# Optimization experiments

Measured on AMD Instinct MI355X. Metric: run time of the kernel, lower is better.

## Reference

```python
import jax, jax.numpy as jnp
import numpy as np

E, S, D_IN, D_LAT, D_HID = 1024, 64, 128, 128, 512
NSTEPS, DT = 8192, 0.01
KL_WEIGHT = 0.01


def setup_inputs() -> dict:
    key = jax.random.key(0)
    ks = jax.random.split(key, 12)
    sd = lambda fan_in: 1.0 / np.sqrt(fan_in)
    return {
        'event_marks': jax.random.normal(ks[0], (E, D_IN), jnp.float32),
        'z_events': jax.random.normal(ks[1], (E, S, D_LAT), jnp.float32),
        'z_traj': jax.random.normal(ks[2], (NSTEPS, S, D_LAT), jnp.float32),
        'times': jnp.arange(NSTEPS + 1, dtype=jnp.float32) * DT,
        'Wp': jax.random.normal(ks[3], (D_IN, D_LAT), jnp.float32) * sd(D_IN),
        'bp': jnp.zeros((D_LAT,), jnp.float32),
        'W1': jax.random.normal(ks[4], (D_LAT, D_HID), jnp.float32) * sd(D_LAT),
        'b1': jnp.zeros((D_HID,), jnp.float32),
        'W2': jax.random.normal(ks[5], (D_HID, 1), jnp.float32) * sd(D_HID),
        'b2': jnp.zeros((1,), jnp.float32),
        'base_intensity': jnp.asarray(0.1, jnp.float32),
        'Wd1': jax.random.normal(ks[6], (D_LAT, D_HID), jnp.float32) * sd(D_LAT),
        'bd1': jnp.zeros((D_HID,), jnp.float32),
        'Wd2': jax.random.normal(ks[7], (D_HID, D_LAT), jnp.float32) * sd(D_HID),
        'bd2': jnp.zeros((D_LAT,), jnp.float32),
    }


def reference(event_marks, z_events, z_traj, times, Wp, bp, W1, b1, W2, b2,
              base_intensity, Wd1, bd1, Wd2, bd2):
    # input projection of marks: [E, D_LAT]
    marks_proj = event_marks @ Wp + bp

    def intensity(z):  # z: [..., D_LAT] -> [...]
        h = jax.nn.relu(z @ W1 + b1)
        s = (h @ W2 + b2)[..., 0]
        return jax.nn.softplus(s + base_intensity)

    # log-intensity at events: sum over events of mean over samples
    lam_ev = intensity(z_events)                      # [E, S]
    log_intensity_sum = jnp.log(lam_ev + 1e-8).mean(axis=1).sum()

    # compensator integral over the trajectory (left Riemann sum)
    lam_traj = intensity(z_traj)                      # [NSTEPS, S]
    dts = jnp.diff(times)                             # [NSTEPS]
    integral = (lam_traj.mean(axis=1) * dts).sum()

    # Gaussian decoder log-prob: mu = MLP(z), unit variance
    h = jax.nn.relu(z_events @ Wd1 + bd1)             # [E, S, D_HID]
    mu = h @ Wd2 + bd2                                # [E, S, D_LAT]
    x = marks_proj[:, None, :]                        # [E, 1, D_LAT]
    log_2pi = jnp.log(jnp.asarray(2.0 * np.pi, jnp.float32))
    log_p = -0.5 * jnp.sum((x - mu) ** 2, axis=-1) - 0.5 * D_LAT * log_2pi  # [E, S]
    recon_loss = log_p.mean(axis=1).sum()

    kl_loss = KL_WEIGHT * jnp.mean(z_traj ** 2)

    elbo = log_intensity_sum - integral + recon_loss - kl_loss
    return -elbo
```

## Files before the change

kernel.cpp:

```cpp
#include <hip/hip_runtime.h>

typedef __attribute__((ext_vector_type(4))) float f32x4;
typedef __attribute__((ext_vector_type(8))) __bf16 bf16x8;
typedef __attribute__((ext_vector_type(4))) __bf16 bf16x4;

#define LOG_2PI 1.8378770664093453f

__device__ __forceinline__ float softplus_f(float x) {
  return fmaxf(x, 0.f) + log1pf(expf(-fabsf(x)));
}

__device__ __forceinline__ void barrier_lds_only() {
  asm volatile("s_waitcnt lgkmcnt(0)\n\ts_barrier" ::: "memory");
}

__global__ void prep_kernel(const float* __restrict__ em,
                            const float* __restrict__ Wp,
                            const float* __restrict__ bp,
                            float* __restrict__ mp,
                            float* __restrict__ accs) {
  const int b = blockIdx.x;
  if (b == 1024) {
    if (threadIdx.x < 8) accs[threadIdx.x] = 0.f;
    return;
  }
  const int d = threadIdx.x;
  float s = bp[d];
  const float* emr = em + b * 128;
#pragma unroll 4
  for (int k = 0; k < 128; ++k) s += emr[k] * Wp[k * 128 + d];
  mp[b * 128 + d] = s;
}

__global__ __launch_bounds__(768, 3) void intensity8_kernel(
    const float* __restrict__ z_traj, const float* __restrict__ z_ev,
    const float* __restrict__ W1, const float* __restrict__ b1,
    const float* __restrict__ W2, const float* __restrict__ b2,
    const float* __restrict__ base_i, const float* __restrict__ times,
    float* __restrict__ accs) {
  __shared__ __align__(16) __bf16 w1t[512 * 128];
  __shared__ __align__(16) float b1L[512];
  __shared__ __align__(16) float w2L[512];
  __shared__ float red[12][4];

  const int tid = threadIdx.x;
  const int wid = tid >> 6, lid = tid & 63;
  const int g = lid >> 4, q = lid & 15;

  if (tid < 512) {
    const float* wcol = W1 + tid;
    char* wb = (char*)w1t;
    const int colbase = tid * 256;
    const int sw = (tid & 7) << 4;
#pragma unroll 8
    for (int k = 0; k < 128; k += 2) {
      float a = wcol[(size_t)k * 512];
      float c = wcol[(size_t)(k + 1) * 512];
      union { __bf16 h[2]; unsigned u; } pk;
      pk.h[0] = (__bf16)a;
      pk.h[1] = (__bf16)c;
      *(unsigned*)(wb + (colbase + ((k * 2) ^ sw))) = pk.u;
    }
    b1L[tid] = b1[tid];
    w2L[tid] = W2[tid];
  }
  const float sbias = b2[0] + base_i[0];
  barrier_lds_only();

  const int gw = blockIdx.x * 12 + wid;
  float integral_loc = 0.f, logsum_loc = 0.f, kls = 0.f;
  const char* wb = (const char*)w1t;
  const int wsw = (q & 7) << 4;

#pragma unroll 1
  for (int p = gw; p < 9216; p += 3072) {
    const bool traj_p = (p < 8192);
    const float* zbase = traj_p ? (z_traj + (size_t)p * 8192)
                                : (z_ev + (size_t)(p - 8192) * 8192);

    bf16x8 fr[4][4];
#pragma unroll
    for (int s = 0; s < 4; ++s) {
      const float* rp = zbase + (s * 16 + q) * 128 + g * 8;
      f32x4 ld[4][2];
#pragma unroll
      for (int kf = 0; kf < 4; ++kf) {
        ld[kf][0] = *(const f32x4*)(rp + kf * 32);
        ld[kf][1] = *(const f32x4*)(rp + kf * 32 + 4);
      }
#pragma unroll
      for (int kf = 0; kf < 4; ++kf) {
        f32x4 a0 = ld[kf][0], a1 = ld[kf][1];
        if (traj_p) {
          kls += a0[0] * a0[0] + a0[1] * a0[1] + a0[2] * a0[2] + a0[3] * a0[3];
          kls += a1[0] * a1[0] + a1[1] * a1[1] + a1[2] * a1[2] + a1[3] * a1[3];
        }
        bf16x8 f;
#pragma unroll
        for (int j = 0; j < 4; ++j) {
          f[j] = (__bf16)a0[j];
          f[4 + j] = (__bf16)a1[j];
        }
        fr[s][kf] = f;
      }
    }

    float rowacc0 = 0.f, rowacc1 = 0.f, rowacc2 = 0.f, rowacc3 = 0.f;
#pragma unroll 2
    for (int c = 0; c < 32; ++c) {
      f32x4 a0 = {}, a1 = {}, a2 = {}, a3 = {};
#pragma unroll
      for (int kf = 0; kf < 4; ++kf) {
        bf16x8 wf = *(const bf16x8*)(wb + c * 4096 + q * 256 +
                                     ((kf * 64 + g * 16) ^ wsw));
        a0 = __builtin_amdgcn_mfma_f32_16x16x32_bf16(wf, fr[0][kf], a0, 0, 0, 0);
        a1 = __builtin_amdgcn_mfma_f32_16x16x32_bf16(wf, fr[1][kf], a1, 0, 0, 0);
        a2 = __builtin_amdgcn_mfma_f32_16x16x32_bf16(wf, fr[2][kf], a2, 0, 0, 0);
        a3 = __builtin_amdgcn_mfma_f32_16x16x32_bf16(wf, fr[3][kf], a3, 0, 0, 0);
      }
      f32x4 bb = *(const f32x4*)&b1L[c * 16 + g * 4];
      f32x4 ww = *(const f32x4*)&w2L[c * 16 + g * 4];
#pragma unroll
      for (int ii = 0; ii < 4; ++ii) {
        rowacc0 += fmaxf(a0[ii] + bb[ii], 0.f) * ww[ii];
        rowacc1 += fmaxf(a1[ii] + bb[ii], 0.f) * ww[ii];
        rowacc2 += fmaxf(a2[ii] + bb[ii], 0.f) * ww[ii];
        rowacc3 += fmaxf(a3[ii] + bb[ii], 0.f) * ww[ii];
      }
    }
    rowacc0 += __shfl_xor(rowacc0, 16);
    rowacc0 += __shfl_xor(rowacc0, 32);
    rowacc1 += __shfl_xor(rowacc1, 16);
    rowacc1 += __shfl_xor(rowacc1, 32);
    rowacc2 += __shfl_xor(rowacc2, 16);
    rowacc2 += __shfl_xor(rowacc2, 32);
    rowacc3 += __shfl_xor(rowacc3, 16);
    rowacc3 += __shfl_xor(rowacc3, 32);

    {
      const int s = lid >> 4;
      const float rs = (s == 0) ? rowacc0 : (s == 1) ? rowacc1
                     : (s == 2) ? rowacc2 : rowacc3;
      const float lam = softplus_f(rs + sbias);
      if (traj_p) {
        integral_loc += lam * (times[p + 1] - times[p]) * (1.f / 64.f);
      } else {
        logsum_loc += logf(lam + 1e-8f) * (1.f / 64.f);
      }
    }
  }

#pragma unroll
  for (int m = 32; m >= 1; m >>= 1) {
    integral_loc += __shfl_xor(integral_loc, m);
    logsum_loc += __shfl_xor(logsum_loc, m);
    kls += __shfl_xor(kls, m);
  }
  if (lid == 0) {
    red[wid][0] = integral_loc;
    red[wid][1] = logsum_loc;
    red[wid][2] = kls;
  }
  __syncthreads();
  if (tid == 0) {
    float I = 0.f, L = 0.f, K = 0.f;
#pragma unroll
    for (int w = 0; w < 12; ++w) {
      I += red[w][0];
      L += red[w][1];
      K += red[w][2];
    }
    atomicAdd(&accs[0], I);
    atomicAdd(&accs[1], L);
    atomicAdd(&accs[3], K);
  }
}

__global__ __launch_bounds__(512, 2) void decoder2_kernel(
    const float* __restrict__ z,
    const float* __restrict__ Wd1, const float* __restrict__ bd1,
    const float* __restrict__ Wd2, const float* __restrict__ bd2,
    const float* __restrict__ mp, float* __restrict__ recon_acc) {
  __shared__ __align__(16) __bf16 zbuf[2][32 * 128];
  __shared__ __align__(16) __bf16 hbuf[32 * 512];
  __shared__ float s_part[32][9];
  __shared__ float red[8];

  const int tid = threadIdx.x;
  const int wid = tid >> 6, lid = tid & 63;
  const int g = lid >> 4, q = lid & 15;
  const int cb = wid * 64;
  const int tile0 = blockIdx.x * 4;

  bf16x8 bw1[4][4];
  f32x4 bd1v[4];
#pragma unroll
  for (int cf = 0; cf < 4; ++cf) {
    const int col = cb + cf * 16 + q;
#pragma unroll
    for (int i = 0; i < 4; ++i) bd1v[cf][i] = bd1[cb + cf * 16 + g * 4 + i];
#pragma unroll
    for (int kf = 0; kf < 4; ++kf) {
      bf16x8 f;
#pragma unroll
      for (int j = 0; j < 8; ++j) f[j] = (__bf16)Wd1[(kf * 32 + g * 8 + j) * 512 + col];
      bw1[cf][kf] = f;
    }
  }
  const int dimf = wid * 16 + q;
  bf16x8 bw2[16];
#pragma unroll
  for (int kf2 = 0; kf2 < 16; ++kf2) {
    bf16x8 f;
#pragma unroll
    for (int j = 0; j < 8; ++j) f[j] = (__bf16)Wd2[(kf2 * 32 + g * 8 + j) * 128 + dimf];
    bw2[kf2] = f;
  }
  f32x4 bd2v;
#pragma unroll
  for (int i = 0; i < 4; ++i) bd2v[i] = bd2[wid * 16 + g * 4 + i];

  const int srow = tid >> 4, sk8 = (tid & 15) * 8;
  const int stg_byte = ((srow * 256 + sk8 * 2) ^ ((srow & 7) << 4));
  char* hb = (char*)hbuf;

  float local = 0.f;

  {
    const float* p = z + (size_t)tile0 * 4096 + tid * 8;
    f32x4 r0 = *(const f32x4*)p, r1 = *(const f32x4*)(p + 4);
    bf16x8 v;
#pragma unroll
    for (int j = 0; j < 4; ++j) { v[j] = (__bf16)r0[j]; v[4 + j] = (__bf16)r1[j]; }
    *(bf16x8*)((char*)zbuf[0] + stg_byte) = v;
  }
  f32x4 rA0, rA1, rB0, rB1;
  { const float* p = z + (size_t)(tile0 + 1) * 4096 + tid * 8; rA0 = *(const f32x4*)p; rA1 = *(const f32x4*)(p + 4); }
  { const float* p = z + (size_t)(tile0 + 2) * 4096 + tid * 8; rB0 = *(const f32x4*)p; rB1 = *(const f32x4*)(p + 4); }
  barrier_lds_only();

#define DBODY(T, ZC, RR0, RR1)                                                     \
  do {                                                                             \
    f32x4 acc1[2][4] = {};                                                         \
    char* zc = (char*)zbuf[ZC];                                                    \
    _Pragma("unroll") for (int kf = 0; kf < 4; ++kf) {                             \
      _Pragma("unroll") for (int rf = 0; rf < 2; ++rf) {                           \
        const int row = rf * 16 + q;                                               \
        bf16x8 a = *(const bf16x8*)(zc + ((row * 256 + kf * 64 + g * 16) ^ ((row & 7) << 4))); \
        _Pragma("unroll") for (int cf = 0; cf < 4; ++cf)                           \
          acc1[rf][cf] = __builtin_amdgcn_mfma_f32_16x16x32_bf16(bw1[cf][kf], a, acc1[rf][cf], 0, 0, 0); \
      }                                                                            \
    }                                                                              \
    {                                                                              \
      bf16x8 v;                                                                    \
      _Pragma("unroll") for (int j = 0; j < 4; ++j) { v[j] = (__bf16)RR0[j]; v[4 + j] = (__bf16)RR1[j]; } \
      *(bf16x8*)((char*)zbuf[(ZC) ^ 1] + stg_byte) = v;                            \
    }                                                                              \
    {                                                                              \
      int tl = (T) + 3; if (tl > 3) tl = 3;                                        \
      const float* p = z + (size_t)(tile0 + tl) * 4096 + tid * 8;                  \
      RR0 = *(const f32x4*)p; RR1 = *(const f32x4*)(p + 4);                        \
    }                                                                              \
    _Pragma("unroll") for (int rf = 0; rf < 2; ++rf) {                             \
      const int row = rf * 16 + q;                                                 \
      _Pragma("unroll") for (int cf = 0; cf < 4; ++cf) {                           \
        bf16x4 hv;                                                                 \
        _Pragma("unroll") for (int i = 0; i < 4; ++i)                              \
          hv[i] = (__bf16)fmaxf(acc1[rf][cf][i] + bd1v[cf][i], 0.f);               \
        const int byt = ((row * 1024 + (cb + cf * 16 + g * 4) * 2) ^ ((row & 7) << 4)); \
        *(bf16x4*)(hb + byt) = hv;                                                 \
      }                                                                            \
    }                                                                              \
    barrier_lds_only();                                                            \
    f32x4 acc2[2] = {};                                                            \
    _Pragma("unroll") for (int kf2 = 0; kf2 < 16; ++kf2) {                         \
      _Pragma("unroll") for (int rf2 = 0; rf2 < 2; ++rf2) {                        \
        const int row = rf2 * 16 + q;                                              \
        bf16x8 a = *(const bf16x8*)(hb + ((row * 1024 + kf2 * 64 + g * 16) ^ ((row & 7) << 4))); \
        acc2[rf2] = __builtin_amdgcn_mfma_f32_16x16x32_bf16(bw2[kf2], a, acc2[rf2], 0, 0, 0); \
      }                                                                            \
    }                                                                              \
    const int e = (tile0 + (T)) >> 1;                                              \
    _Pragma("unroll") for (int rf2 = 0; rf2 < 2; ++rf2) {                          \
      float partial = 0.f;                                                         \
      _Pragma("unroll") for (int i = 0; i < 4; ++i) {                              \
        const float xv = mp[e * 128 + wid * 16 + g * 4 + i];                       \
        const float d = xv - (acc2[rf2][i] + bd2v[i]);                             \
        partial += d * d;                                                          \
      }                                                                            \
      partial += __shfl_xor(partial, 16);                                          \
      partial += __shfl_xor(partial, 32);                                          \
      if (lid < 16) s_part[rf2 * 16 + lid][wid] = partial;                         \
    }                                                                              \
    barrier_lds_only();                                                            \
    if (tid < 32) {                                                                \
      float t2 = 0.f;                                                              \
      _Pragma("unroll") for (int w = 0; w < 8; ++w) t2 += s_part[tid][w];          \
      local += (-0.5f * t2 - 0.5f * 128.f * LOG_2PI) * (1.f / 64.f);               \
    }                                                                              \
  } while (0)

#pragma unroll 1
  for (int t = 0; t < 4; t += 2) {
    DBODY(t, 0, rA0, rA1);
    DBODY(t + 1, 1, rB0, rB1);
  }
#undef DBODY

  if (wid == 0) {
#pragma unroll
    for (int m = 16; m >= 1; m >>= 1) local += __shfl_xor(local, m);
    if (lid == 0) atomicAdd(recon_acc, local);
  }
}

__global__ void finalize_kernel(const float* __restrict__ accs, float* __restrict__ out) {
  const float kl = 0.01f * (accs[3] / 67108864.f);
  const float elbo = accs[1] - accs[0] + accs[2] - kl;
  out[0] = -elbo;
}

extern "C" void kernel_launch(void* const* d_in, const int* in_sizes, int n_in,
                              void* d_out, int out_size, void* d_ws, size_t ws_size,
                              hipStream_t stream) {
  const float* event_marks = (const float*)d_in[0];
  const float* z_events = (const float*)d_in[1];
  const float* z_traj = (const float*)d_in[2];
  const float* times = (const float*)d_in[3];
  const float* Wp = (const float*)d_in[4];
  const float* bp = (const float*)d_in[5];
  const float* W1 = (const float*)d_in[6];
  const float* b1 = (const float*)d_in[7];
  const float* W2 = (const float*)d_in[8];
  const float* b2 = (const float*)d_in[9];
  const float* base_i = (const float*)d_in[10];
  const float* Wd1 = (const float*)d_in[11];
  const float* bd1 = (const float*)d_in[12];
  const float* Wd2 = (const float*)d_in[13];
  const float* bd2 = (const float*)d_in[14];

  float* mp = (float*)d_ws;
  float* accs = (float*)((char*)d_ws + 1024 * 128 * 4);

  prep_kernel<<<1025, 128, 0, stream>>>(event_marks, Wp, bp, mp, accs);
  intensity8_kernel<<<256, 768, 0, stream>>>(z_traj, z_events, W1, b1, W2, b2,
                                             base_i, times, accs);
  decoder2_kernel<<<512, 512, 0, stream>>>(z_events, Wd1, bd1, Wd2, bd2, mp,
                                           &accs[2]);
  finalize_kernel<<<1, 1, 0, stream>>>(accs, (float*)d_out);
}
```

Measured before the change: 148.3 us.

## Prefetch next z tile into registers while computing current intensity tile

The intensity kernel drops from 12 to 8 waves per block, and the work is remapped so each wave handles four trajectory tiles plus an event tile on alternate waves. Registers are double-buffered so the next tile's global loads are issued before the MFMA loop on the current tile. The first tile's load is also issued before the W1 staging into LDS, hiding that latency. The cost is 32 extra f32x4 registers per lane, fewer resident waves, and an uneven 5-versus-4 round split across waves.

Measured after the change: 187.5 us. 26.5% more time.

```diff
diff --git a/kernel.cpp b/kernel.cpp
--- a/kernel.cpp
+++ b/kernel.cpp
@@ -32,7 +32,7 @@
   mp[b * 128 + d] = s;
 }
 
-__global__ __launch_bounds__(768, 3) void intensity8_kernel(
+__global__ __launch_bounds__(512, 2) void intensity9_kernel(
     const float* __restrict__ z_traj, const float* __restrict__ z_ev,
     const float* __restrict__ W1, const float* __restrict__ b1,
     const float* __restrict__ W2, const float* __restrict__ b2,
@@ -41,15 +41,34 @@
   __shared__ __align__(16) __bf16 w1t[512 * 128];
   __shared__ __align__(16) float b1L[512];
   __shared__ __align__(16) float w2L[512];
-  __shared__ float red[12][4];
+  __shared__ float red[8][4];
 
   const int tid = threadIdx.x;
   const int wid = tid >> 6, lid = tid & 63;
   const int g = lid >> 4, q = lid & 15;
-
-  if (tid < 512) {
+  const int gw = blockIdx.x * 8 + wid;
+  const int nrounds = (gw & 1) ? 4 : 5;
+
+  f32x4 stg[4][4][2];
+
+#define ZPTR(P) ((P) < 8192 ? z_traj + (size_t)(P) * 8192 \
+                            : z_ev + (size_t)((P) - 8192) * 8192)
+#define LOADP(ZP)                                                          \
+  do {                                                                     \
+    _Pragma("unroll") for (int s = 0; s < 4; ++s) {                        \
+      const float* rp = (ZP) + (s * 16 + q) * 128 + g * 8;                 \
+      _Pragma("unroll") for (int kf = 0; kf < 4; ++kf) {                   \
+        stg[s][kf][0] = *(const f32x4*)(rp + kf * 32);                     \
+        stg[s][kf][1] = *(const f32x4*)(rp + kf * 32 + 4);                 \
+      }                                                                    \
+    }                                                                      \
+  } while (0)
+
+  LOADP(ZPTR(gw));
+
+  {
     const float* wcol = W1 + tid;
-    char* wb = (char*)w1t;
+    char* wbs = (char*)w1t;
     const int colbase = tid * 256;
     const int sw = (tid & 7) << 4;
 #pragma unroll 8
@@ -59,7 +78,7 @@
       union { __bf16 h[2]; unsigned u; } pk;
       pk.h[0] = (__bf16)a;
       pk.h[1] = (__bf16)c;
-      *(unsigned*)(wb + (colbase + ((k * 2) ^ sw))) = pk.u;
+      *(unsigned*)(wbs + (colbase + ((k * 2) ^ sw))) = pk.u;
     }
     b1L[tid] = b1[tid];
     w2L[tid] = W2[tid];
@@ -67,31 +86,22 @@
   const float sbias = b2[0] + base_i[0];
   barrier_lds_only();
 
-  const int gw = blockIdx.x * 12 + wid;
   float integral_loc = 0.f, logsum_loc = 0.f, kls = 0.f;
   const char* wb = (const char*)w1t;
   const int wsw = (q & 7) << 4;
 
 #pragma unroll 1
-  for (int p = gw; p < 9216; p += 3072) {
-    const bool traj_p = (p < 8192);
-    const float* zbase = traj_p ? (z_traj + (size_t)p * 8192)
-                                : (z_ev + (size_t)(p - 8192) * 8192);
+  for (int r = 0; r < nrounds; ++r) {
+    const bool traj_r = (r < 4);
+    const int p = traj_r ? r * 2048 + gw : 8192 + (gw >> 1);
 
     bf16x8 fr[4][4];
 #pragma unroll
     for (int s = 0; s < 4; ++s) {
-      const float* rp = zbase + (s * 16 + q) * 128 + g * 8;
-      f32x4 ld[4][2];
 #pragma unroll
       for (int kf = 0; kf < 4; ++kf) {
-        ld[kf][0] = *(const f32x4*)(rp + kf * 32);
-        ld[kf][1] = *(const f32x4*)(rp + kf * 32 + 4);
-      }
-#pragma unroll
-      for (int kf = 0; kf < 4; ++kf) {
-        f32x4 a0 = ld[kf][0], a1 = ld[kf][1];
-        if (traj_p) {
+        f32x4 a0 = stg[s][kf][0], a1 = stg[s][kf][1];
+        if (traj_r) {
           kls += a0[0] * a0[0] + a0[1] * a0[1] + a0[2] * a0[2] + a0[3] * a0[3];
           kls += a1[0] * a1[0] + a1[1] * a1[1] + a1[2] * a1[2] + a1[3] * a1[3];
         }
@@ -104,6 +114,13 @@
         fr[s][kf] = f;
       }
     }
+
+    if (r + 1 < nrounds) {
+      const int pn = (r + 1 < 4) ? (r + 1) * 2048 + gw : 8192 + (gw >> 1);
+      const float* zn = ZPTR(pn);
+      LOADP(zn);
+    }
+    __builtin_amdgcn_sched_barrier(0);
 
     float rowacc0 = 0.f, rowacc1 = 0.f, rowacc2 = 0.f, rowacc3 = 0.f;
 #pragma unroll 2
@@ -142,13 +159,15 @@
       const float rs = (s == 0) ? rowacc0 : (s == 1) ? rowacc1
                      : (s == 2) ? rowacc2 : rowacc3;
       const float lam = softplus_f(rs + sbias);
-      if (traj_p) {
+      if (traj_r) {
         integral_loc += lam * (times[p + 1] - times[p]) * (1.f / 64.f);
       } else {
         logsum_loc += logf(lam + 1e-8f) * (1.f / 64.f);
       }
     }
   }
+#undef LOADP
+#undef ZPTR
 
 #pragma unroll
   for (int m = 32; m >= 1; m >>= 1) {
@@ -165,7 +184,7 @@
   if (tid == 0) {
     float I = 0.f, L = 0.f, K = 0.f;
 #pragma unroll
-    for (int w = 0; w < 12; ++w) {
+    for (int w = 0; w < 8; ++w) {
       I += red[w][0];
       L += red[w][1];
       K += red[w][2];
@@ -343,7 +362,7 @@
   float* accs = (float*)((char*)d_ws + 1024 * 128 * 4);
 
   prep_kernel<<<1025, 128, 0, stream>>>(event_marks, Wp, bp, mp, accs);
-  intensity8_kernel<<<256, 768, 0, stream>>>(z_traj, z_events, W1, b1, W2, b2,
+  intensity9_kernel<<<256, 512, 0, stream>>>(z_traj, z_events, W1, b1, W2, b2,
                                              base_i, times, accs);
   decoder2_kernel<<<512, 512, 0, stream>>>(z_events, Wd1, bd1, Wd2, bd2, mp,
                                            &accs[2]);
```

## Fuse mark projection into intensity kernel, fold bias into MFMA, halve decoder tiles

Applied to the files above, without the earlier changes.

Removes the separate prep kernel: the marks projection now runs in 171 extra blocks appended to the intensity kernel's grid, and the accumulators are zeroed with a memset. In the intensity loop the b1 bias is used as the MFMA accumulator's initial value, and b1/W2 are read from global memory instead of LDS. The decoder now handles 2 tiles per block over 1024 blocks, dropping the multi-tile prefetch pipeline for more parallelism. The aim is less launch overhead and better occupancy, at the cost of losing prefetch overlap in the decoder and adding global loads in the hot loop.

Result: slower. 176.3 us (+18.9%).

```diff
diff --git a/kernel.cpp b/kernel.cpp
--- a/kernel.cpp
+++ b/kernel.cpp
@@ -14,42 +14,39 @@
   asm volatile("s_waitcnt lgkmcnt(0)\n\ts_barrier" ::: "memory");
 }
 
-__global__ void prep_kernel(const float* __restrict__ em,
-                            const float* __restrict__ Wp,
-                            const float* __restrict__ bp,
-                            float* __restrict__ mp,
-                            float* __restrict__ accs) {
-  const int b = blockIdx.x;
-  if (b == 1024) {
-    if (threadIdx.x < 8) accs[threadIdx.x] = 0.f;
-    return;
-  }
-  const int d = threadIdx.x;
-  float s = bp[d];
-  const float* emr = em + b * 128;
-#pragma unroll 4
-  for (int k = 0; k < 128; ++k) s += emr[k] * Wp[k * 128 + d];
-  mp[b * 128 + d] = s;
-}
-
-__global__ __launch_bounds__(768, 3) void intensity8_kernel(
+__global__ __launch_bounds__(768, 3) void intensity13_kernel(
     const float* __restrict__ z_traj, const float* __restrict__ z_ev,
     const float* __restrict__ W1, const float* __restrict__ b1,
     const float* __restrict__ W2, const float* __restrict__ b2,
     const float* __restrict__ base_i, const float* __restrict__ times,
+    const float* __restrict__ em, const float* __restrict__ Wp,
+    const float* __restrict__ bp, float* __restrict__ mp,
     float* __restrict__ accs) {
   __shared__ __align__(16) __bf16 w1t[512 * 128];
-  __shared__ __align__(16) float b1L[512];
-  __shared__ __align__(16) float w2L[512];
   __shared__ float red[12][4];
 
   const int tid = threadIdx.x;
+
+  if (blockIdx.x >= 256) {
+    const int e = (blockIdx.x - 256) * 6 + (tid >> 7);
+    if (e < 1024) {
+      const int d = tid & 127;
+      float s = bp[d];
+      const float* emr = em + e * 128;
+#pragma unroll 4
+      for (int k = 0; k < 128; ++k) s += emr[k] * Wp[k * 128 + d];
+      mp[e * 128 + d] = s;
+    }
+    return;
+  }
+
   const int wid = tid >> 6, lid = tid & 63;
   const int g = lid >> 4, q = lid & 15;
+  const int gw = blockIdx.x * 12 + wid;
 
   if (tid < 512) {
     const float* wcol = W1 + tid;
-    char* wb = (char*)w1t;
+    char* wbs = (char*)w1t;
     const int colbase = tid * 256;
     const int sw = (tid & 7) << 4;
 #pragma unroll 8
@@ -59,15 +56,12 @@
       union { __bf16 h[2]; unsigned u; } pk;
       pk.h[0] = (__bf16)a;
       pk.h[1] = (__bf16)c;
-      *(unsigned*)(wb + (colbase + ((k * 2) ^ sw))) = pk.u;
-    }
-    b1L[tid] = b1[tid];
-    w2L[tid] = W2[tid];
+      *(unsigned*)(wbs + (colbase + ((k * 2) ^ sw))) = pk.u;
+    }
   }
   const float sbias = b2[0] + base_i[0];
   barrier_lds_only();
 
-  const int gw = blockIdx.x * 12 + wid;
   float integral_loc = 0.f, logsum_loc = 0.f, kls = 0.f;
   const char* wb = (const char*)w1t;
   const int wsw = (q & 7) << 4;
@@ -108,7 +102,10 @@
     float rowacc0 = 0.f, rowacc1 = 0.f, rowacc2 = 0.f, rowacc3 = 0.f;
 #pragma unroll 2
     for (int c = 0; c < 32; ++c) {
-      f32x4 a0 = {}, a1 = {}, a2 = {}, a3 = {};
+      const int c0 = c * 16 + g * 4;
+      f32x4 bb = *(const f32x4*)&b1[c0];
+      f32x4 ww = *(const f32x4*)&W2[c0];
+      f32x4 a0 = bb, a1 = bb, a2 = bb, a3 = bb;
 #pragma unroll
       for (int kf = 0; kf < 4; ++kf) {
         bf16x8 wf = *(const bf16x8*)(wb + c * 4096 + q * 256 +
@@ -118,14 +115,12 @@
         a2 = __builtin_amdgcn_mfma_f32_16x16x32_bf16(wf, fr[2][kf], a2, 0, 0, 0);
         a3 = __builtin_amdgcn_mfma_f32_16x16x32_bf16(wf, fr[3][kf], a3, 0, 0, 0);
       }
-      f32x4 bb = *(const f32x4*)&b1L[c * 16 + g * 4];
-      f32x4 ww = *(const f32x4*)&w2L[c * 16 + g * 4];
 #pragma unroll
       for (int ii = 0; ii < 4; ++ii) {
-        rowacc0 += fmaxf(a0[ii] + bb[ii], 0.f) * ww[ii];
-        rowacc1 += fmaxf(a1[ii] + bb[ii], 0.f) * ww[ii];
-        rowacc2 += fmaxf(a2[ii] + bb[ii], 0.f) * ww[ii];
-        rowacc3 += fmaxf(a3[ii] + bb[ii], 0.f) * ww[ii];
+        rowacc0 += fmaxf(a0[ii], 0.f) * ww[ii];
+        rowacc1 += fmaxf(a1[ii], 0.f) * ww[ii];
+        rowacc2 += fmaxf(a2[ii], 0.f) * ww[ii];
+        rowacc3 += fmaxf(a3[ii], 0.f) * ww[ii];
       }
     }
     rowacc0 += __shfl_xor(rowacc0, 16);
@@ -176,7 +171,7 @@
   }
 }
 
-__global__ __launch_bounds__(512, 2) void decoder2_kernel(
+__global__ __launch_bounds__(512, 2) void decoder3_kernel(
     const float* __restrict__ z,
     const float* __restrict__ Wd1, const float* __restrict__ bd1,
     const float* __restrict__ Wd2, const float* __restrict__ bd2,
@@ -190,7 +185,7 @@
   const int wid = tid >> 6, lid = tid & 63;
   const int g = lid >> 4, q = lid & 15;
   const int cb = wid * 64;
-  const int tile0 = blockIdx.x * 4;
+  const int tile0 = blockIdx.x * 2;
 
   bf16x8 bw1[4][4];
   f32x4 bd1v[4];
@@ -234,15 +229,18 @@
     for (int j = 0; j < 4; ++j) { v[j] = (__bf16)r0[j]; v[4 + j] = (__bf16)r1[j]; }
     *(bf16x8*)((char*)zbuf[0] + stg_byte) = v;
   }
-  f32x4 rA0, rA1, rB0, rB1;
-  { const float* p = z + (size_t)(tile0 + 1) * 4096 + tid * 8; rA0 = *(const f32x4*)p; rA1 = *(const f32x4*)(p + 4); }
-  { const float* p = z + (size_t)(tile0 + 2) * 4096 + tid * 8; rB0 = *(const f32x4*)p; rB1 = *(const f32x4*)(p + 4); }
+  f32x4 rA0, rA1;
+  {
+    const float* p = z + (size_t)(tile0 + 1) * 4096 + tid * 8;
+    rA0 = *(const f32x4*)p;
+    rA1 = *(const f32x4*)(p + 4);
+  }
   barrier_lds_only();
 
-#define DBODY(T, ZC, RR0, RR1)                                                     \
+#define DBODY(T, DO_STAGE)                                                         \
   do {                                                                             \
     f32x4 acc1[2][4] = {};                                                         \
-    char* zc = (char*)zbuf[ZC];                                                    \
+    char* zc = (char*)zbuf[(T)];                                                   \
     _Pragma("unroll") for (int kf = 0; kf < 4; ++kf) {                             \
       _Pragma("unroll") for (int rf = 0; rf < 2; ++rf) {                           \
         const int row = rf * 16 + q;                                               \
@@ -251,15 +249,10 @@
           acc1[rf][cf] = __builtin_amdgcn_mfma_f32_16x16x32_bf16(bw1[cf][kf], a, acc1[rf][cf], 0, 0, 0); \
       }                                                                            \
     }                                                                              \
-    {                                                                              \
+    if (DO_STAGE) {                                                                \
       bf16x8 v;                                                                    \
-      _Pragma("unroll") for (int j = 0; j < 4; ++j) { v[j] = (__bf16)RR0[j]; v[4 + j] = (__bf16)RR1[j]; } \
-      *(bf16x8*)((char*)zbuf[(ZC) ^ 1] + stg_byte) = v;                            \
-    }                                                                              \
-    {                                                                              \
-      int tl = (T) + 3; if (tl > 3) tl = 3;                                        \
-      const float* p = z + (size_t)(tile0 + tl) * 4096 + tid * 8;                  \
-      RR0 = *(const f32x4*)p; RR1 = *(const f32x4*)(p + 4);                        \
+      _Pragma("unroll") for (int j = 0; j < 4; ++j) { v[j] = (__bf16)rA0[j]; v[4 + j] = (__bf16)rA1[j]; } \
+      *(bf16x8*)((char*)zbuf[1] + stg_byte) = v;                                   \
     }                                                                              \
     _Pragma("unroll") for (int rf = 0; rf < 2; ++rf) {                             \
       const int row = rf * 16 + q;                                                 \
@@ -298,13 +291,11 @@
       _Pragma("unroll") for (int w = 0; w < 8; ++w) t2 += s_part[tid][w];          \
       local += (-0.5f * t2 - 0.5f * 128.f * LOG_2PI) * (1.f / 64.f);               \
     }                                                                              \
+    barrier_lds_only();                                                            \
   } while (0)
 
-#pragma unroll 1
-  for (int t = 0; t < 4; t += 2) {
-    DBODY(t, 0, rA0, rA1);
-    DBODY(t + 1, 1, rB0, rB1);
-  }
+  DBODY(0, true);
+  DBODY(1, false);
 #undef DBODY
 
   if (wid == 0) {
@@ -342,10 +333,11 @@
   float* mp = (float*)d_ws;
   float* accs = (float*)((char*)d_ws + 1024 * 128 * 4);
 
-  prep_kernel<<<1025, 128, 0, stream>>>(event_marks, Wp, bp, mp, accs);
-  intensity8_kernel<<<256, 768, 0, stream>>>(z_traj, z_events, W1, b1, W2, b2,
-                                             base_i, times, accs);
-  decoder2_kernel<<<512, 512, 0, stream>>>(z_events, Wd1, bd1, Wd2, bd2, mp,
-                                           &accs[2]);
+  (void)hipMemsetAsync(accs, 0, 4 * sizeof(float), stream);
+  intensity13_kernel<<<427, 768, 0, stream>>>(z_traj, z_events, W1, b1, W2, b2,
+                                              base_i, times, event_marks, Wp,
+                                              bp, mp, accs);
+  decoder3_kernel<<<1024, 512, 0, stream>>>(z_events, Wd1, bd1, Wd2, bd2, mp,
+                                            &accs[2]);
   finalize_kernel<<<1, 1, 0, stream>>>(accs, (float*)d_out);
 }
```

## Widen intensity warp tiles to 96 rows and double decoder tiles per block

Applied to the files above, without the earlier changes.

The intensity kernel now processes flat 96-row tiles that span the trajectory and event tensors. Each LDS-loaded W1 fragment feeds six MFMAs instead of four, and each warp runs two loop iterations instead of three. The decoder kernel handles 8 tiles per block with half as many blocks, and gains an extra LDS barrier per tile to protect the shared partial buffer. The wider tile raises register pressure (more fragments and accumulators, with the inner unroll reduced to 1), which may cause spills. Halving the decoder grid may also leave compute units underused.

After: 208.6 us. 40.7% more time.

```diff
diff --git a/kernel.cpp b/kernel.cpp
--- a/kernel.cpp
+++ b/kernel.cpp
@@ -32,7 +32,7 @@
   mp[b * 128 + d] = s;
 }
 
-__global__ __launch_bounds__(768, 3) void intensity8_kernel(
+__global__ __launch_bounds__(768, 3) void intensity15_kernel(
     const float* __restrict__ z_traj, const float* __restrict__ z_ev,
     const float* __restrict__ W1, const float* __restrict__ b1,
     const float* __restrict__ W2, const float* __restrict__ b2,
@@ -49,7 +49,7 @@
 
   if (tid < 512) {
     const float* wcol = W1 + tid;
-    char* wb = (char*)w1t;
+    char* wbs = (char*)w1t;
     const int colbase = tid * 256;
     const int sw = (tid & 7) << 4;
 #pragma unroll 8
@@ -59,7 +59,7 @@
       union { __bf16 h[2]; unsigned u; } pk;
       pk.h[0] = (__bf16)a;
       pk.h[1] = (__bf16)c;
-      *(unsigned*)(wb + (colbase + ((k * 2) ^ sw))) = pk.u;
+      *(unsigned*)(wbs + (colbase + ((k * 2) ^ sw))) = pk.u;
     }
     b1L[tid] = b1[tid];
     w2L[tid] = W2[tid];
@@ -73,15 +73,15 @@
   const int wsw = (q & 7) << 4;
 
 #pragma unroll 1
-  for (int p = gw; p < 9216; p += 3072) {
-    const bool traj_p = (p < 8192);
-    const float* zbase = traj_p ? (z_traj + (size_t)p * 8192)
-                                : (z_ev + (size_t)(p - 8192) * 8192);
-
-    bf16x8 fr[4][4];
-#pragma unroll
-    for (int s = 0; s < 4; ++s) {
-      const float* rp = zbase + (s * 16 + q) * 128 + g * 8;
+  for (int t = gw; t < 6144; t += 3072) {
+    bf16x8 fr[6][4];
+#pragma unroll
+    for (int s = 0; s < 6; ++s) {
+      const int row = t * 96 + s * 16 + q;
+      const bool tr = (row < 524288);
+      const float* rp =
+          (tr ? z_traj + (size_t)row * 128 : z_ev + (size_t)(row - 524288) * 128) +
+          g * 8;
       f32x4 ld[4][2];
 #pragma unroll
       for (int kf = 0; kf < 4; ++kf) {
@@ -91,7 +91,7 @@
 #pragma unroll
       for (int kf = 0; kf < 4; ++kf) {
         f32x4 a0 = ld[kf][0], a1 = ld[kf][1];
-        if (traj_p) {
+        if (tr) {
           kls += a0[0] * a0[0] + a0[1] * a0[1] + a0[2] * a0[2] + a0[3] * a0[3];
           kls += a1[0] * a1[0] + a1[1] * a1[1] + a1[2] * a1[2] + a1[3] * a1[3];
         }
@@ -105,10 +105,10 @@
       }
     }
 
-    float rowacc0 = 0.f, rowacc1 = 0.f, rowacc2 = 0.f, rowacc3 = 0.f;
-#pragma unroll 2
+    float ra0 = 0.f, ra1 = 0.f, ra2 = 0.f, ra3 = 0.f, ra4 = 0.f, ra5 = 0.f;
+#pragma unroll 1
     for (int c = 0; c < 32; ++c) {
-      f32x4 a0 = {}, a1 = {}, a2 = {}, a3 = {};
+      f32x4 a0 = {}, a1 = {}, a2 = {}, a3 = {}, a4 = {}, a5 = {};
 #pragma unroll
       for (int kf = 0; kf < 4; ++kf) {
         bf16x8 wf = *(const bf16x8*)(wb + c * 4096 + q * 256 +
@@ -117,33 +117,46 @@
         a1 = __builtin_amdgcn_mfma_f32_16x16x32_bf16(wf, fr[1][kf], a1, 0, 0, 0);
         a2 = __builtin_amdgcn_mfma_f32_16x16x32_bf16(wf, fr[2][kf], a2, 0, 0, 0);
         a3 = __builtin_amdgcn_mfma_f32_16x16x32_bf16(wf, fr[3][kf], a3, 0, 0, 0);
+        a4 = __builtin_amdgcn_mfma_f32_16x16x32_bf16(wf, fr[4][kf], a4, 0, 0, 0);
+        a5 = __builtin_amdgcn_mfma_f32_16x16x32_bf16(wf, fr[5][kf], a5, 0, 0, 0);
       }
       f32x4 bb = *(const f32x4*)&b1L[c * 16 + g * 4];
       f32x4 ww = *(const f32x4*)&w2L[c * 16 + g * 4];
 #pragma unroll
       for (int ii = 0; ii < 4; ++ii) {
-        rowacc0 += fmaxf(a0[ii] + bb[ii], 0.f) * ww[ii];
-        rowacc1 += fmaxf(a1[ii] + bb[ii], 0.f) * ww[ii];
-        rowacc2 += fmaxf(a2[ii] + bb[ii], 0.f) * ww[ii];
-        rowacc3 += fmaxf(a3[ii] + bb[ii], 0.f) * ww[ii];
-      }
-    }
-    rowacc0 += __shfl_xor(rowacc0, 16);
-    rowacc0 += __shfl_xor(rowacc0, 32);
-    rowacc1 += __shfl_xor(rowacc1, 16);
-    rowacc1 += __shfl_xor(rowacc1, 32);
-    rowacc2 += __shfl_xor(rowacc2, 16);
-    rowacc2 += __shfl_xor(rowacc2, 32);
-    rowacc3 += __shfl_xor(rowacc3, 16);
-    rowacc3 += __shfl_xor(rowacc3, 32);
+        ra0 += fmaxf(a0[ii] + bb[ii], 0.f) * ww[ii];
+        ra1 += fmaxf(a1[ii] + bb[ii], 0.f) * ww[ii];
+        ra2 += fmaxf(a2[ii] + bb[ii], 0.f) * ww[ii];
+        ra3 += fmaxf(a3[ii] + bb[ii], 0.f) * ww[ii];
+        ra4 += fmaxf(a4[ii] + bb[ii], 0.f) * ww[ii];
+        ra5 += fmaxf(a5[ii] + bb[ii], 0.f) * ww[ii];
+      }
+    }
+    ra0 += __shfl_xor(ra0, 16); ra0 += __shfl_xor(ra0, 32);
+    ra1 += __shfl_xor(ra1, 16); ra1 += __shfl_xor(ra1, 32);
+    ra2 += __shfl_xor(ra2, 16); ra2 += __shfl_xor(ra2, 32);
+    ra3 += __shfl_xor(ra3, 16); ra3 += __shfl_xor(ra3, 32);
+    ra4 += __shfl_xor(ra4, 16); ra4 += __shfl_xor(ra4, 32);
+    ra5 += __shfl_xor(ra5, 16); ra5 += __shfl_xor(ra5, 32);
 
     {
-      const int s = lid >> 4;
-      const float rs = (s == 0) ? rowacc0 : (s == 1) ? rowacc1
-                     : (s == 2) ? rowacc2 : rowacc3;
+      const float rs = (g == 0) ? ra0 : (g == 1) ? ra1 : (g == 2) ? ra2 : ra3;
+      const int row = t * 96 + g * 16 + q;
       const float lam = softplus_f(rs + sbias);
-      if (traj_p) {
-        integral_loc += lam * (times[p + 1] - times[p]) * (1.f / 64.f);
+      if (row < 524288) {
+        const int ts = row >> 6;
+        integral_loc += lam * (times[ts + 1] - times[ts]) * (1.f / 64.f);
+      } else {
+        logsum_loc += logf(lam + 1e-8f) * (1.f / 64.f);
+      }
+    }
+    if (g < 2) {
+      const float rs = (g == 0) ? ra4 : ra5;
+      const int row = t * 96 + (4 + g) * 16 + q;
+      const float lam = softplus_f(rs + sbias);
+      if (row < 524288) {
+        const int ts = row >> 6;
+        integral_loc += lam * (times[ts + 1] - times[ts]) * (1.f / 64.f);
       } else {
         logsum_loc += logf(lam + 1e-8f) * (1.f / 64.f);
       }
@@ -190,7 +203,7 @@
   const int wid = tid >> 6, lid = tid & 63;
   const int g = lid >> 4, q = lid & 15;
   const int cb = wid * 64;
-  const int tile0 = blockIdx.x * 4;
+  const int tile0 = blockIdx.x * 8;
 
   bf16x8 bw1[4][4];
   f32x4 bd1v[4];
@@ -257,7 +270,7 @@
       *(bf16x8*)((char*)zbuf[(ZC) ^ 1] + stg_byte) = v;                            \
     }                                                                              \
     {                                                                              \
-      int tl = (T) + 3; if (tl > 3) tl = 3;                                        \
+      int tl = (T) + 3; if (tl > 7) tl = 7;                                        \
       const float* p = z + (size_t)(tile0 + tl) * 4096 + tid * 8;                  \
       RR0 = *(const f32x4*)p; RR1 = *(const f32x4*)(p + 4);                        \
     }                                                                              \
@@ -298,10 +311,11 @@
       _Pragma("unroll") for (int w = 0; w < 8; ++w) t2 += s_part[tid][w];          \
       local += (-0.5f * t2 - 0.5f * 128.f * LOG_2PI) * (1.f / 64.f);               \
     }                                                                              \
+    barrier_lds_only();                                                            \
   } while (0)
 
 #pragma unroll 1
-  for (int t = 0; t < 4; t += 2) {
+  for (int t = 0; t < 8; t += 2) {
     DBODY(t, 0, rA0, rA1);
     DBODY(t + 1, 1, rB0, rB1);
   }
@@ -343,9 +357,9 @@
   float* accs = (float*)((char*)d_ws + 1024 * 128 * 4);
 
   prep_kernel<<<1025, 128, 0, stream>>>(event_marks, Wp, bp, mp, accs);
-  intensity8_kernel<<<256, 768, 0, stream>>>(z_traj, z_events, W1, b1, W2, b2,
-                                             base_i, times, accs);
-  decoder2_kernel<<<512, 512, 0, stream>>>(z_events, Wd1, bd1, Wd2, bd2, mp,
+  intensity15_kernel<<<256, 768, 0, stream>>>(z_traj, z_events, W1, b1, W2, b2,
+                                              base_i, times, accs);
+  decoder2_kernel<<<256, 512, 0, stream>>>(z_events, Wd1, bd1, Wd2, bd2, mp,
                                            &accs[2]);
   finalize_kernel<<<1, 1, 0, stream>>>(accs, (float*)d_out);
 }
```
